# Kernel tuning notes

Measured on AMD Instinct MI355X. Metric: run time of the kernel, lower is better.

The kernel has to match this reference:

```python
import jax, jax.numpy as jnp
import numpy as np

B, N, D = 2048, 64, 128  # batch, num hist nodes (n-1), d_model
EPS = 1e-8


def setup_inputs() -> dict:
    key = jax.random.key(0)
    k1, k2, k3, k4, k5 = jax.random.split(key, 5)
    A_guide = jax.random.uniform(k1, (B, N, N), dtype=jnp.float32)  # nonneg for NMF
    X_guide = jax.random.normal(k2, (B, D, N), dtype=jnp.float32)
    x_new = jax.random.normal(k3, (B, 1, D), dtype=jnp.float32)
    U0 = jax.random.normal(k4, (B, N, N), dtype=jnp.float32)  # pre-softplus NMF init
    V0 = jax.random.normal(k5, (B, N, N), dtype=jnp.float32)
    return {"A_guide": A_guide, "X_guide": X_guide, "x_new": x_new, "U0": U0, "V0": V0}


def _nmf(A, U0, V0, n_iter=10):
    U = jax.nn.softplus(U0)
    V = jax.nn.softplus(V0)

    def step(carry, _):
        U, V = carry
        UT = jnp.swapaxes(U, 1, 2)
        V = V * (UT @ A) / (UT @ U @ V + EPS)
        VT = jnp.swapaxes(V, 1, 2)
        U = U * (A @ VT) / (U @ V @ VT + EPS)
        return (U, V), None

    (U, V), _ = jax.lax.scan(step, (U, V), None, length=n_iter)
    return U, V


def reference(A_guide, X_guide, x_new, U0, V0):
    d_model = X_guide.shape[1]
    n = X_guide.shape[2]
    # Step 1: deterministic NMF of historical adjacency
    U, V = _nmf(A_guide, U0, V0)
    # Step 2: orthogonal projection P = X X^T  (B, d, d)
    P = X_guide @ jnp.swapaxes(X_guide, 1, 2)
    # project new node feature: (B,1,d) @ (B,d,d) -> (B,d)
    x_p = (x_new @ P)[:, 0]
    # semantic attention: (B,1,n)
    attn_semantic = jnp.einsum('bd,bdn->bn', x_p, X_guide) / (d_model ** 0.5)
    # structural attention via UV reconstruction
    a = U @ V                                      # (B, n, n)
    x_p_rep = jnp.broadcast_to(x_p[:, None, :], (x_p.shape[0], n, x_p.shape[1]))
    x_p_UV = a @ x_p_rep                           # (B, n, d)
    attn_struct = x_p_UV @ X_guide                 # (B, n, n)
    fused = attn_semantic[:, None, :] * attn_struct  # broadcast (B,1,n)*(B,n,n)
    A_Tn = jax.nn.softmax(fused, axis=-1)
    return (A_Tn, x_p, U, V)
```

## Files before the change

kernel.cpp:

```cpp
#include <hip/hip_runtime.h>
#include <hip/hip_bf16.h>

#define EPS 1e-8f

typedef _Float16 half8 __attribute__((ext_vector_type(8)));
typedef _Float16 half4 __attribute__((ext_vector_type(4)));
typedef float f32x4 __attribute__((ext_vector_type(4)));

__device__ __forceinline__ float softplus_f(float x) {
    return fmaxf(x, 0.f) + log1pf(expf(-fabsf(x)));
}

__device__ __forceinline__ int swzh(int r, int c) {
    return r * 64 + ((((c >> 3) ^ (r & 7)) << 3) | (c & 7));
}

struct Frag {
    half8 h0, h1;
};

__device__ __forceinline__ Frag load_frag(const _Float16* B, int i, int lr, int lk) {
    const int row = i * 16 + lr;
    const int x = lr & 7;
    Frag f;
    f.h0 = *(const half8*)(B + row * 64 + ((lk ^ x) << 3));
    f.h1 = *(const half8*)(B + row * 64 + (((lk + 4) ^ x) << 3));
    return f;
}

__device__ __forceinline__ void mfma_acc(const Frag& a, const Frag& b, f32x4& acc) {
    acc = __builtin_amdgcn_mfma_f32_16x16x32_f16(a.h0, b.h0, acc, 0, 0, 0);
    acc = __builtin_amdgcn_mfma_f32_16x16x32_f16(a.h1, b.h1, acc, 0, 0, 0);
}

struct NmfLds {
    _Float16 U_rm[4096];
    _Float16 U_cm[4096];
    _Float16 V_rm[4096];
    _Float16 V_cm[4096];
    union {
        _Float16 WZ[4096];
        float vp[4][64];
    } u;
};

__global__ __launch_bounds__(256, 4) void nmf_kernel(const float* __restrict__ Ag,
                                                     const float* __restrict__ U0,
                                                     const float* __restrict__ V0,
                                                     float* __restrict__ out,
                                                     float* __restrict__ ws) {
    __shared__ NmfLds S;
    const int b = blockIdx.x;
    const int tid = threadIdx.x;
    const int wave = tid >> 6;
    const int lane = tid & 63;
    const int lr = lane & 15;
    const int lk = lane >> 4;

    const float* Ab = Ag + (size_t)b * 4096;
    const float* Ub = U0 + (size_t)b * 4096;
    const float* Vb = V0 + (size_t)b * 4096;

    float Ureg[4][4];
    float VregT[4][4];

#pragma unroll
    for (int t = 0; t < 4; ++t)
#pragma unroll
        for (int q = 0; q < 4; ++q) {
            const int r = wave * 16 + lk * 4 + q;
            const int c = t * 16 + lr;
            float a = Ab[r * 64 + c];
            S.U_rm[swzh(r, c)] = (_Float16)a;
            S.U_cm[swzh(c, r)] = (_Float16)a;
        }
    __syncthreads();
    const Frag arm = load_frag(S.U_rm, wave, lr, lk);
    const Frag acm = load_frag(S.U_cm, wave, lr, lk);
    __syncthreads();

#pragma unroll
    for (int t = 0; t < 4; ++t)
#pragma unroll
        for (int q = 0; q < 4; ++q) {
            const int r = wave * 16 + lk * 4 + q;
            const int c = t * 16 + lr;
            float uv = softplus_f(Ub[r * 64 + c]);
            Ureg[t][q] = uv;
            S.U_rm[swzh(r, c)] = (_Float16)uv;
            S.U_cm[swzh(c, r)] = (_Float16)uv;
            float vv = softplus_f(Vb[c * 64 + r]);
            VregT[t][q] = vv;
            S.V_cm[swzh(r, c)] = (_Float16)vv;
            S.V_rm[swzh(c, r)] = (_Float16)vv;
        }
    __syncthreads();

    const f32x4 zero4 = {0.f, 0.f, 0.f, 0.f};

    for (int it = 0; it < 10; ++it) {
        Frag ucself = load_frag(S.U_cm, wave, lr, lk);
        f32x4 T1T[4] = {zero4, zero4, zero4, zero4};
        f32x4 W[4] = {zero4, zero4, zero4, zero4};
#pragma unroll
        for (int ct = 0; ct < 4; ++ct) {
            Frag uct = load_frag(S.U_cm, ct, lr, lk);
            mfma_acc(acm, uct, T1T[ct]);
            mfma_acc(ucself, uct, W[ct]);
        }
#pragma unroll
        for (int t = 0; t < 4; ++t) {
            half4 p = {(_Float16)W[t][0], (_Float16)W[t][1], (_Float16)W[t][2],
                       (_Float16)W[t][3]};
            *(half4*)(&S.u.WZ[swzh(t * 16 + lr, wave * 16 + lk * 4)]) = p;
        }
        __syncthreads();

        Frag vtself = load_frag(S.V_cm, wave, lr, lk);
        f32x4 WVT[4] = {zero4, zero4, zero4, zero4};
#pragma unroll
        for (int ct = 0; ct < 4; ++ct) {
            Frag wct = load_frag(S.u.WZ, ct, lr, lk);
            mfma_acc(vtself, wct, WVT[ct]);
        }

#pragma unroll
        for (int t = 0; t < 4; ++t) {
            half4 p;
#pragma unroll
            for (int q = 0; q < 4; ++q) {
                float v =
                    VregT[t][q] * T1T[t][q] * __builtin_amdgcn_rcpf(WVT[t][q] + EPS);
                VregT[t][q] = v;
                _Float16 h = (_Float16)v;
                p[q] = h;
                S.V_cm[swzh(wave * 16 + lk * 4 + q, t * 16 + lr)] = h;
            }
            *(half4*)(&S.V_rm[swzh(t * 16 + lr, wave * 16 + lk * 4)]) = p;
        }
        __syncthreads();

        Frag vrself = load_frag(S.V_rm, wave, lr, lk);
        f32x4 T2[4] = {zero4, zero4, zero4, zero4};
        f32x4 Y[4] = {zero4, zero4, zero4, zero4};
#pragma unroll
        for (int ct = 0; ct < 4; ++ct) {
            Frag vct = load_frag(S.V_rm, ct, lr, lk);
            mfma_acc(arm, vct, T2[ct]);
            mfma_acc(vrself, vct, Y[ct]);
        }
#pragma unroll
        for (int t = 0; t < 4; ++t) {
            half4 p = {(_Float16)Y[t][0], (_Float16)Y[t][1], (_Float16)Y[t][2],
                       (_Float16)Y[t][3]};
            *(half4*)(&S.u.WZ[swzh(t * 16 + lr, wave * 16 + lk * 4)]) = p;
        }
        __syncthreads();

        Frag urself = load_frag(S.U_rm, wave, lr, lk);
        f32x4 ZV[4] = {zero4, zero4, zero4, zero4};
#pragma unroll
        for (int ct = 0; ct < 4; ++ct) {
            Frag yct = load_frag(S.u.WZ, ct, lr, lk);
            mfma_acc(urself, yct, ZV[ct]);
        }

#pragma unroll
        for (int t = 0; t < 4; ++t) {
            half4 p;
#pragma unroll
            for (int q = 0; q < 4; ++q) {
                float u = Ureg[t][q] * T2[t][q] * __builtin_amdgcn_rcpf(ZV[t][q] + EPS);
                Ureg[t][q] = u;
                _Float16 h = (_Float16)u;
                p[q] = h;
                S.U_rm[swzh(wave * 16 + lk * 4 + q, t * 16 + lr)] = h;
            }
            *(half4*)(&S.U_cm[swzh(t * 16 + lr, wave * 16 + lk * 4)]) = p;
        }
        __syncthreads();
    }

    {
        float part[4];
#pragma unroll
        for (int t = 0; t < 4; ++t) {
            float s = VregT[t][0] + VregT[t][1] + VregT[t][2] + VregT[t][3];
            s += __shfl_xor(s, 16);
            s += __shfl_xor(s, 32);
            part[t] = s;
        }
        if (lk == 0) {
#pragma unroll
            for (int t = 0; t < 4; ++t) S.u.vp[wave][t * 16 + lr] = part[t];
        }
    }
    __syncthreads();
#pragma unroll
    for (int q = 0; q < 4; ++q) {
        float p = 0.f;
#pragma unroll
        for (int t = 0; t < 4; ++t) {
            float vs = S.u.vp[0][t * 16 + lr] + S.u.vp[1][t * 16 + lr] +
                       S.u.vp[2][t * 16 + lr] + S.u.vp[3][t * 16 + lr];
            p += Ureg[t][q] * vs;
        }
        p += __shfl_xor(p, 1);
        p += __shfl_xor(p, 2);
        p += __shfl_xor(p, 4);
        p += __shfl_xor(p, 8);
        if (lr == 0) ws[(size_t)b * 64 + wave * 16 + lk * 4 + q] = p;
    }

    {
        float* Uout = out + 8650752 + (size_t)b * 4096;
        float* Vout = out + 17039360 + (size_t)b * 4096;
        const int rr = tid >> 2, qt = tid & 3;
        const _Float16* Up = S.U_rm + swzh(rr, qt * 16);
        const _Float16* Vp = S.V_rm + swzh(rr, qt * 16);
        half8 u0 = *(const half8*)(Up);
        half8 u1 = *(const half8*)(S.U_rm + swzh(rr, qt * 16 + 8));
        half8 v0 = *(const half8*)(Vp);
        half8 v1 = *(const half8*)(S.V_rm + swzh(rr, qt * 16 + 8));
        float4* Uo = (float4*)(Uout + rr * 64 + qt * 16);
        float4* Vo = (float4*)(Vout + rr * 64 + qt * 16);
        Uo[0] = {(float)u0[0], (float)u0[1], (float)u0[2], (float)u0[3]};
        Uo[1] = {(float)u0[4], (float)u0[5], (float)u0[6], (float)u0[7]};
        Uo[2] = {(float)u1[0], (float)u1[1], (float)u1[2], (float)u1[3]};
        Uo[3] = {(float)u1[4], (float)u1[5], (float)u1[6], (float)u1[7]};
        Vo[0] = {(float)v0[0], (float)v0[1], (float)v0[2], (float)v0[3]};
        Vo[1] = {(float)v0[4], (float)v0[5], (float)v0[6], (float)v0[7]};
        Vo[2] = {(float)v1[0], (float)v1[1], (float)v1[2], (float)v1[3]};
        Vo[3] = {(float)v1[4], (float)v1[5], (float)v1[6], (float)v1[7]};
    }
}

__global__ __launch_bounds__(256) void xp_kernel(const float* __restrict__ Xg,
                                                 const float* __restrict__ xn,
                                                 float* __restrict__ out,
                                                 float* __restrict__ ws) {
    __shared__ float X[128 * 65];
    __shared__ float xnew[128];
    __shared__ float red[256];
    __shared__ float tbuf[64];
    __shared__ float xp[128];
    const int b = blockIdx.x, tid = threadIdx.x;
    const float* Xb = Xg + (size_t)b * 8192;

    for (int idx = tid; idx < 2048; idx += 256) {
        float4 v = ((const float4*)Xb)[idx];
        int d = idx >> 4, n = (idx * 4) & 63;
        X[d * 65 + n + 0] = v.x;
        X[d * 65 + n + 1] = v.y;
        X[d * 65 + n + 2] = v.z;
        X[d * 65 + n + 3] = v.w;
    }
    if (tid < 32) {
        float4 v = ((const float4*)(xn + (size_t)b * 128))[tid];
        xnew[tid * 4 + 0] = v.x;
        xnew[tid * 4 + 1] = v.y;
        xnew[tid * 4 + 2] = v.z;
        xnew[tid * 4 + 3] = v.w;
    }
    __syncthreads();
    {
        const int n = tid & 63, g = tid >> 6;
        float p = 0.f;
        for (int d = g * 32; d < g * 32 + 32; ++d) p += xnew[d] * X[d * 65 + n];
        red[g * 64 + n] = p;
    }
    __syncthreads();
    if (tid < 64) tbuf[tid] = red[tid] + red[64 + tid] + red[128 + tid] + red[192 + tid];
    __syncthreads();
    {
        const int d = tid & 127, h = tid >> 7;
        float p = 0.f;
        for (int n = h * 32; n < h * 32 + 32; ++n) p += X[d * 65 + n] * tbuf[n];
        red[h * 128 + d] = p;
    }
    __syncthreads();
    if (tid < 128) {
        float v = red[tid] + red[128 + tid];
        xp[tid] = v;
        out[8388608 + (size_t)b * 128 + tid] = v;
    }
    __syncthreads();
    {
        const int n = tid & 63, g = tid >> 6;
        float p = 0.f;
        for (int d = g * 32; d < g * 32 + 32; ++d) p += xp[d] * X[d * 65 + n];
        red[g * 64 + n] = p;
    }
    __syncthreads();
    if (tid < 64)
        ws[131072 + (size_t)b * 64 + tid] =
            red[tid] + red[64 + tid] + red[128 + tid] + red[192 + tid];
}

__global__ __launch_bounds__(256) void fuse_kernel(const float* __restrict__ ws,
                                                   float* __restrict__ out) {
    __shared__ float g[64];
    __shared__ float rs[64];
    __shared__ float gmax_s;
    const int b = blockIdx.x, tid = threadIdx.x;
    if (tid < 64) {
        float s = ws[131072 + (size_t)b * 64 + tid];
        g[tid] = s * s * 0.088388347648318447f;
        rs[tid] = ws[(size_t)b * 64 + tid];
    }
    __syncthreads();
    if (tid < 64) {
        float m = g[tid];
#pragma unroll
        for (int o = 1; o < 64; o <<= 1) m = fmaxf(m, __shfl_xor(m, o));
        if (tid == 0) gmax_s = m;
    }
    __syncthreads();
    const float gmax = gmax_s;
    const int i = tid >> 2, part = tid & 3;
    const float r = rs[i];
    float e[16];
    float sum = 0.f;
#pragma unroll
    for (int j = 0; j < 16; ++j) {
        e[j] = expf(r * (g[part * 16 + j] - gmax));
        sum += e[j];
    }
    sum += __shfl_xor(sum, 1);
    sum += __shfl_xor(sum, 2);
    const float inv = 1.f / sum;
    float* o = out + (size_t)b * 4096 + i * 64 + part * 16;
#pragma unroll
    for (int j = 0; j < 16; j += 4) {
        float4 v = {e[j] * inv, e[j + 1] * inv, e[j + 2] * inv, e[j + 3] * inv};
        ((float4*)o)[j >> 2] = v;
    }
}

extern "C" void kernel_launch(void* const* d_in, const int* in_sizes, int n_in,
                              void* d_out, int out_size, void* d_ws, size_t ws_size,
                              hipStream_t stream) {
    (void)in_sizes; (void)n_in; (void)out_size; (void)ws_size;
    const float* Ag = (const float*)d_in[0];
    const float* Xg = (const float*)d_in[1];
    const float* xn = (const float*)d_in[2];
    const float* U0 = (const float*)d_in[3];
    const float* V0 = (const float*)d_in[4];
    float* out = (float*)d_out;
    float* ws = (float*)d_ws;

    hipLaunchKernelGGL(nmf_kernel, dim3(2048), dim3(256), 0, stream, Ag, U0, V0, out, ws);
    hipLaunchKernelGGL(xp_kernel, dim3(2048), dim3(256), 0, stream, Xg, xn, out, ws);
    hipLaunchKernelGGL(fuse_kernel, dim3(2048), dim3(256), 0, stream, ws, out);
}
```

Measured before the change: 159.3 us.

## Fuse softmax kernel into xp kernel and precompute swizzled LDS addresses in NMF

Merges the fuse (softmax) kernel into the xp kernel, so the semantic scores stay in shared memory and the NMF row sums are read directly, removing one launch and a workspace round trip. In the NMF kernel, the swizzled LDS fragment and store addresses are hoisted into per-thread base pointers with compile-time strip offsets, and V_cm is reordered in the LDS struct. This cuts per-iteration index arithmetic, at the cost of more live registers for the precomputed pointers.

```diff
diff --git a/kernel.cpp b/kernel.cpp
--- a/kernel.cpp
+++ b/kernel.cpp
@@ -19,12 +19,11 @@
     half8 h0, h1;
 };
 
-__device__ __forceinline__ Frag load_frag(const _Float16* B, int i, int lr, int lk) {
-    const int row = i * 16 + lr;
-    const int x = lr & 7;
+template <int CT>
+__device__ __forceinline__ Frag load_strip(const _Float16* p0, const _Float16* p1) {
     Frag f;
-    f.h0 = *(const half8*)(B + row * 64 + ((lk ^ x) << 3));
-    f.h1 = *(const half8*)(B + row * 64 + (((lk + 4) ^ x) << 3));
+    f.h0 = *(const half8*)(p0 + CT * 1024);
+    f.h1 = *(const half8*)(p1 + CT * 1024);
     return f;
 }
 
@@ -34,10 +33,10 @@
 }
 
 struct NmfLds {
+    _Float16 V_cm[4096];
     _Float16 U_rm[4096];
     _Float16 U_cm[4096];
     _Float16 V_rm[4096];
-    _Float16 V_cm[4096];
     union {
         _Float16 WZ[4096];
         float vp[4][64];
@@ -56,6 +55,7 @@
     const int lane = tid & 63;
     const int lr = lane & 15;
     const int lk = lane >> 4;
+    const int x = lr & 7;
 
     const float* Ab = Ag + (size_t)b * 4096;
     const float* Ub = U0 + (size_t)b * 4096;
@@ -63,6 +63,34 @@
 
     float Ureg[4][4];
     float VregT[4][4];
+
+    const int sg0 = (lk ^ x) << 3;
+    const int sg1 = ((lk + 4) ^ x) << 3;
+    const _Float16* rUcm0 = S.U_cm + lr * 64 + sg0;
+    const _Float16* rUcm1 = S.U_cm + lr * 64 + sg1;
+    const _Float16* rVrm0 = S.V_rm + lr * 64 + sg0;
+    const _Float16* rVrm1 = S.V_rm + lr * 64 + sg1;
+    const _Float16* rWZ0 = S.u.WZ + lr * 64 + sg0;
+    const _Float16* rWZ1 = S.u.WZ + lr * 64 + sg1;
+    const int srow = (wave * 16 + lr) * 64;
+    const _Float16* sUrm0 = S.U_rm + srow + sg0;
+    const _Float16* sUrm1 = S.U_rm + srow + sg1;
+    const _Float16* sUcm0 = S.U_cm + srow + sg0;
+    const _Float16* sUcm1 = S.U_cm + srow + sg1;
+    const _Float16* sVcm0 = S.V_cm + srow + sg0;
+    const _Float16* sVcm1 = S.V_cm + srow + sg1;
+    const _Float16* sVrm0 = S.V_rm + srow + sg0;
+    const _Float16* sVrm1 = S.V_rm + srow + sg1;
+    const int cg = ((wave * 2 + (lk >> 1)) ^ x) << 3;
+    const int bg = (lk & 1) << 2;
+    _Float16* wtrV = S.V_rm + lr * 64 + cg + bg;
+    _Float16* wtrU = S.U_cm + lr * 64 + cg + bg;
+    _Float16* wtrW = S.u.WZ + lr * 64 + cg + bg;
+    const int g0 = lr >> 3;
+    int oq[4];
+#pragma unroll
+    for (int q = 0; q < 4; ++q)
+        oq[q] = (wave * 16 + lk * 4 + q) * 64 + ((g0 ^ ((lk * 4 + q) & 7)) << 3) + x;
 
 #pragma unroll
     for (int t = 0; t < 4; ++t)
@@ -75,8 +103,8 @@
             S.U_cm[swzh(c, r)] = (_Float16)a;
         }
     __syncthreads();
-    const Frag arm = load_frag(S.U_rm, wave, lr, lk);
-    const Frag acm = load_frag(S.U_cm, wave, lr, lk);
+    const Frag arm = load_strip<0>(sUrm0, sUrm1);
+    const Frag acm = load_strip<0>(sUcm0, sUcm1);
     __syncthreads();
 
 #pragma unroll
@@ -99,30 +127,32 @@
     const f32x4 zero4 = {0.f, 0.f, 0.f, 0.f};
 
     for (int it = 0; it < 10; ++it) {
-        Frag ucself = load_frag(S.U_cm, wave, lr, lk);
+        Frag ucself = load_strip<0>(sUcm0, sUcm1);
         f32x4 T1T[4] = {zero4, zero4, zero4, zero4};
         f32x4 W[4] = {zero4, zero4, zero4, zero4};
-#pragma unroll
-        for (int ct = 0; ct < 4; ++ct) {
-            Frag uct = load_frag(S.U_cm, ct, lr, lk);
-            mfma_acc(acm, uct, T1T[ct]);
-            mfma_acc(ucself, uct, W[ct]);
-        }
+#define S1STEP(CT)                                \
+    {                                             \
+        Frag uct = load_strip<CT>(rUcm0, rUcm1);  \
+        mfma_acc(acm, uct, T1T[CT]);              \
+        mfma_acc(ucself, uct, W[CT]);             \
+    }
+        S1STEP(0) S1STEP(1) S1STEP(2) S1STEP(3)
 #pragma unroll
         for (int t = 0; t < 4; ++t) {
             half4 p = {(_Float16)W[t][0], (_Float16)W[t][1], (_Float16)W[t][2],
                        (_Float16)W[t][3]};
-            *(half4*)(&S.u.WZ[swzh(t * 16 + lr, wave * 16 + lk * 4)]) = p;
+            *(half4*)(wtrW + t * 1024) = p;
         }
         __syncthreads();
 
-        Frag vtself = load_frag(S.V_cm, wave, lr, lk);
+        Frag vtself = load_strip<0>(sVcm0, sVcm1);
         f32x4 WVT[4] = {zero4, zero4, zero4, zero4};
-#pragma unroll
-        for (int ct = 0; ct < 4; ++ct) {
-            Frag wct = load_frag(S.u.WZ, ct, lr, lk);
-            mfma_acc(vtself, wct, WVT[ct]);
-        }
+#define S2STEP(CT)                               \
+    {                                            \
+        Frag wct = load_strip<CT>(rWZ0, rWZ1);   \
+        mfma_acc(vtself, wct, WVT[CT]);          \
+    }
+        S2STEP(0) S2STEP(1) S2STEP(2) S2STEP(3)
 
 #pragma unroll
         for (int t = 0; t < 4; ++t) {
@@ -134,36 +164,38 @@
                 VregT[t][q] = v;
                 _Float16 h = (_Float16)v;
                 p[q] = h;
-                S.V_cm[swzh(wave * 16 + lk * 4 + q, t * 16 + lr)] = h;
+                S.V_cm[oq[q] ^ (t << 4)] = h;
             }
-            *(half4*)(&S.V_rm[swzh(t * 16 + lr, wave * 16 + lk * 4)]) = p;
+            *(half4*)(wtrV + t * 1024) = p;
         }
         __syncthreads();
 
-        Frag vrself = load_frag(S.V_rm, wave, lr, lk);
+        Frag vrself = load_strip<0>(sVrm0, sVrm1);
         f32x4 T2[4] = {zero4, zero4, zero4, zero4};
         f32x4 Y[4] = {zero4, zero4, zero4, zero4};
-#pragma unroll
-        for (int ct = 0; ct < 4; ++ct) {
-            Frag vct = load_frag(S.V_rm, ct, lr, lk);
-            mfma_acc(arm, vct, T2[ct]);
-            mfma_acc(vrself, vct, Y[ct]);
-        }
+#define S4STEP(CT)                                \
+    {                                             \
+        Frag vct = load_strip<CT>(rVrm0, rVrm1);  \
+        mfma_acc(arm, vct, T2[CT]);               \
+        mfma_acc(vrself, vct, Y[CT]);             \
+    }
+        S4STEP(0) S4STEP(1) S4STEP(2) S4STEP(3)
 #pragma unroll
         for (int t = 0; t < 4; ++t) {
             half4 p = {(_Float16)Y[t][0], (_Float16)Y[t][1], (_Float16)Y[t][2],
                        (_Float16)Y[t][3]};
-            *(half4*)(&S.u.WZ[swzh(t * 16 + lr, wave * 16 + lk * 4)]) = p;
+            *(half4*)(wtrW + t * 1024) = p;
         }
         __syncthreads();
 
-        Frag urself = load_frag(S.U_rm, wave, lr, lk);
+        Frag urself = load_strip<0>(sUrm0, sUrm1);
         f32x4 ZV[4] = {zero4, zero4, zero4, zero4};
-#pragma unroll
-        for (int ct = 0; ct < 4; ++ct) {
-            Frag yct = load_frag(S.u.WZ, ct, lr, lk);
-            mfma_acc(urself, yct, ZV[ct]);
-        }
+#define S5STEP(CT)                              \
+    {                                           \
+        Frag yct = load_strip<CT>(rWZ0, rWZ1);  \
+        mfma_acc(urself, yct, ZV[CT]);          \
+    }
+        S5STEP(0) S5STEP(1) S5STEP(2) S5STEP(3)
 
 #pragma unroll
         for (int t = 0; t < 4; ++t) {
@@ -174,9 +206,9 @@
                 Ureg[t][q] = u;
                 _Float16 h = (_Float16)u;
                 p[q] = h;
-                S.U_rm[swzh(wave * 16 + lk * 4 + q, t * 16 + lr)] = h;
+                S.U_rm[oq[q] ^ (t << 4)] = h;
             }
-            *(half4*)(&S.U_cm[swzh(t * 16 + lr, wave * 16 + lk * 4)]) = p;
+            *(half4*)(wtrU + t * 1024) = p;
         }
         __syncthreads();
     }
@@ -216,11 +248,9 @@
         float* Uout = out + 8650752 + (size_t)b * 4096;
         float* Vout = out + 17039360 + (size_t)b * 4096;
         const int rr = tid >> 2, qt = tid & 3;
-        const _Float16* Up = S.U_rm + swzh(rr, qt * 16);
-        const _Float16* Vp = S.V_rm + swzh(rr, qt * 16);
-        half8 u0 = *(const half8*)(Up);
+        half8 u0 = *(const half8*)(S.U_rm + swzh(rr, qt * 16));
         half8 u1 = *(const half8*)(S.U_rm + swzh(rr, qt * 16 + 8));
-        half8 v0 = *(const half8*)(Vp);
+        half8 v0 = *(const half8*)(S.V_rm + swzh(rr, qt * 16));
         half8 v1 = *(const half8*)(S.V_rm + swzh(rr, qt * 16 + 8));
         float4* Uo = (float4*)(Uout + rr * 64 + qt * 16);
         float4* Vo = (float4*)(Vout + rr * 64 + qt * 16);
@@ -238,12 +268,15 @@
 __global__ __launch_bounds__(256) void xp_kernel(const float* __restrict__ Xg,
                                                  const float* __restrict__ xn,
                                                  float* __restrict__ out,
-                                                 float* __restrict__ ws) {
+                                                 const float* __restrict__ ws) {
     __shared__ float X[128 * 65];
     __shared__ float xnew[128];
     __shared__ float red[256];
     __shared__ float tbuf[64];
     __shared__ float xp[128];
+    __shared__ float g[64];
+    __shared__ float rs[64];
+    __shared__ float gmax_s;
     const int b = blockIdx.x, tid = threadIdx.x;
     const float* Xb = Xg + (size_t)b * 8192;
 
@@ -262,12 +295,13 @@
         xnew[tid * 4 + 2] = v.z;
         xnew[tid * 4 + 3] = v.w;
     }
-    __syncthreads();
-    {
-        const int n = tid & 63, g = tid >> 6;
+    if (tid >= 192) rs[tid - 192] = ws[(size_t)b * 64 + tid - 192];
+    __syncthreads();
+    {
+        const int n = tid & 63, gi = tid >> 6;
         float p = 0.f;
-        for (int d = g * 32; d < g * 32 + 32; ++d) p += xnew[d] * X[d * 65 + n];
-        red[g * 64 + n] = p;
+        for (int d = gi * 32; d < gi * 32 + 32; ++d) p += xnew[d] * X[d * 65 + n];
+        red[gi * 64 + n] = p;
     }
     __syncthreads();
     if (tid < 64) tbuf[tid] = red[tid] + red[64 + tid] + red[128 + tid] + red[192 + tid];
@@ -286,27 +320,15 @@
     }
     __syncthreads();
     {
-        const int n = tid & 63, g = tid >> 6;
+        const int n = tid & 63, gi = tid >> 6;
         float p = 0.f;
-        for (int d = g * 32; d < g * 32 + 32; ++d) p += xp[d] * X[d * 65 + n];
-        red[g * 64 + n] = p;
-    }
-    __syncthreads();
-    if (tid < 64)
-        ws[131072 + (size_t)b * 64 + tid] =
-            red[tid] + red[64 + tid] + red[128 + tid] + red[192 + tid];
-}
-
-__global__ __launch_bounds__(256) void fuse_kernel(const float* __restrict__ ws,
-                                                   float* __restrict__ out) {
-    __shared__ float g[64];
-    __shared__ float rs[64];
-    __shared__ float gmax_s;
-    const int b = blockIdx.x, tid = threadIdx.x;
+        for (int d = gi * 32; d < gi * 32 + 32; ++d) p += xp[d] * X[d * 65 + n];
+        red[gi * 64 + n] = p;
+    }
+    __syncthreads();
     if (tid < 64) {
-        float s = ws[131072 + (size_t)b * 64 + tid];
+        float s = red[tid] + red[64 + tid] + red[128 + tid] + red[192 + tid];
         g[tid] = s * s * 0.088388347648318447f;
-        rs[tid] = ws[(size_t)b * 64 + tid];
     }
     __syncthreads();
     if (tid < 64) {
@@ -351,5 +373,4 @@
 
     hipLaunchKernelGGL(nmf_kernel, dim3(2048), dim3(256), 0, stream, Ag, U0, V0, out, ws);
     hipLaunchKernelGGL(xp_kernel, dim3(2048), dim3(256), 0, stream, Xg, xn, out, ws);
-    hipLaunchKernelGGL(fuse_kernel, dim3(2048), dim3(256), 0, stream, ws, out);
-}
+}
```

New measurement: 155.5 us, median of 2. 1.02x faster.
